# Performance work log

Measured on AMD Instinct MI355X. Metric: run time of the kernel, lower is better.

Reference implementation:

```python
import jax, jax.numpy as jnp
import numpy as np
from jax import lax

B, C, H, W = 8, 64, 128, 128
KS = 3          # kernel size
K = KS * KS     # kernel field = 9
PAD = 1


def conv2d(x, w, b):
    # x: [B,Cin,H,W], w: [Cout,Cin,kh,kw], 'same' 3x3 conv
    y = lax.conv_general_dilated(x, w, window_strides=(1, 1),
                                 padding=((PAD, PAD), (PAD, PAD)),
                                 dimension_numbers=('NCHW', 'OIHW', 'NCHW'))
    return y + b[None, :, None, None]


def modulated_deform_conv(x, offset, mask, weight, bias):
    # x:[B,C,H,W], offset:[B,2K,H,W] (dy,dx per tap), mask:[B,K,H,W]
    Bs, Cin, Hin, Win = x.shape
    off = offset.reshape(Bs, K, 2, Hin, Win)
    ky, kx = jnp.meshgrid(jnp.arange(KS), jnp.arange(KS), indexing='ij')
    ky = ky.reshape(K).astype(x.dtype)   # kernel tap row offsets 0..2
    kx = kx.reshape(K).astype(x.dtype)
    # sampling positions p = p0 + p_k + offset (stride=1, pad=1)
    py = (jnp.arange(Hin, dtype=x.dtype)[None, None, :, None] - PAD
          + ky[None, :, None, None] + off[:, :, 0])            # [B,K,H,W]
    px = (jnp.arange(Win, dtype=x.dtype)[None, None, None, :] - PAD
          + kx[None, :, None, None] + off[:, :, 1])            # [B,K,H,W]

    y0 = jnp.floor(py); x0 = jnp.floor(px)
    ly = py - y0; lx = px - x0                                  # frac parts
    y0i = y0.astype(jnp.int32); x0i = x0.astype(jnp.int32)

    x_flat = x.reshape(Bs, Cin, Hin * Win)

    def gather(iy, ix):
        valid = ((iy >= 0) & (iy < Hin) & (ix >= 0) & (ix < Win))
        flat = (jnp.clip(iy, 0, Hin - 1) * Win + jnp.clip(ix, 0, Win - 1))
        g = jax.vmap(lambda xb, ib: xb[:, ib])(x_flat, flat.reshape(Bs, -1))
        g = g.reshape(Bs, Cin, K, Hin, Win)
        return g * valid[:, None].astype(x.dtype)

    w00 = ((1 - ly) * (1 - lx))[:, None]  # [B,1,K,H,W]
    w01 = ((1 - ly) * lx)[:, None]
    w10 = (ly * (1 - lx))[:, None]
    w11 = (ly * lx)[:, None]

    val = (w00 * gather(y0i, x0i) + w01 * gather(y0i, x0i + 1)
           + w10 * gather(y0i + 1, x0i) + w11 * gather(y0i + 1, x0i + 1))
    val = val * mask[:, None]                                   # modulation
    out = jnp.einsum('ock,bckhw->bohw', weight.reshape(weight.shape[0], Cin, K), val)
    return out + bias[None, :, None, None]


def setup_inputs() -> dict:
    key = jax.random.key(0)
    ks = jax.random.split(key, 7)
    s = 0.05
    return {
        'x': jax.random.normal(ks[0], (B, C, H, W), jnp.float32),
        'w_om': jax.random.normal(ks[1], (3 * K, C, KS, KS), jnp.float32) * s,
        'b_om': jax.random.normal(ks[2], (3 * K,), jnp.float32) * s,
        'w_dc': jax.random.normal(ks[3], (C, C, KS, KS), jnp.float32) * s,
        'b_dc': jax.random.normal(ks[4], (C,), jnp.float32) * s,
        'w_c': jax.random.normal(ks[5], (C, C, KS, KS), jnp.float32) * s,
        'b_c': jax.random.normal(ks[6], (C,), jnp.float32) * s,
    }


def reference(x, w_om, b_om, w_dc, b_dc, w_c, b_c):
    om = conv2d(x, w_om, b_om)                       # [B,3K,H,W]
    offset, mask_raw = om[:, :2 * K], om[:, 2 * K:]
    mask = 2.0 * jax.nn.sigmoid(mask_raw)
    out = modulated_deform_conv(x, offset, mask, w_dc, b_dc)
    act = jnp.where(out > 0, out, 0.2 * out)         # LeakyReLU(0.2)
    return conv2d(act, w_c, b_c) + x
```

## Files before the change

### kernel.cpp

```cpp
#include <hip/hip_runtime.h>
#include <math.h>

#define Bn 8
#define Cn 64
#define Hn 128
#define Wn 128
#define HWn (Hn * Wn)
#define Kn 9

typedef __attribute__((ext_vector_type(8))) short short8;
typedef __attribute__((ext_vector_type(4))) float floatx4;

__device__ __forceinline__ float bf2f(short s) {
  return __uint_as_float(((unsigned)(unsigned short)s) << 16);
}
__device__ __forceinline__ short f2bf(float f) {
  unsigned u = __float_as_uint(f);
  u += 0x7fff + ((u >> 16) & 1);
  return (short)(u >> 16);
}

__global__ __launch_bounds__(256) void k_prep_w(
    const float* __restrict__ w_om, const float* __restrict__ w_dc,
    const float* __restrict__ w_c, short* __restrict__ wt) {
  int idx = blockIdx.x * 256 + threadIdx.x;
  if (idx >= 160 * 576) return;
  int row = idx / 576, k = idx - row * 576;
  int kk = k >> 6, cin = k & 63;
  float v;
  if (row < 32)
    v = (row < 27) ? w_om[(row * 64 + cin) * 9 + kk] : 0.f;
  else if (row < 96)
    v = w_dc[((row - 32) * 64 + cin) * 9 + kk];
  else
    v = w_c[((row - 96) * 64 + cin) * 9 + kk];
  wt[idx] = f2bf(v);
}

__global__ __launch_bounds__(256) void k_prep_x(const float* __restrict__ x,
                                                short* __restrict__ xT) {
  __shared__ float tile[64][129];
  const int h = blockIdx.x, b = blockIdx.y;
  const int tid = threadIdx.x;
  const float* xb = x + (size_t)b * 64 * HWn + h * Wn;
  for (int i = tid; i < 8192; i += 256) {
    int c = i >> 7, w = i & 127;
    tile[c][w] = xb[c * HWn + w];
  }
  __syncthreads();
  short* dst = xT + ((size_t)(b * Hn + h) * Wn) * 64;
  for (int i = tid; i < 2048; i += 256) {
    int w = i >> 4, c4 = (i & 15) * 4;
    short4 o;
    o.x = f2bf(tile[c4 + 0][w]);
    o.y = f2bf(tile[c4 + 1][w]);
    o.z = f2bf(tile[c4 + 2][w]);
    o.w = f2bf(tile[c4 + 3][w]);
    *(short4*)(dst + (size_t)w * 64 + c4) = o;
  }
}

__global__ __launch_bounds__(256) void k_conv_om(
    const short* __restrict__ xT, const short* __restrict__ wt_om,
    const float* __restrict__ b_om, float* __restrict__ offmask) {
  __shared__ short val[64][296];
  const int b = blockIdx.z, h = blockIdx.y, w0 = blockIdx.x * 64;
  const int tid = threadIdx.x;
  const int wave = tid >> 6, lane = tid & 63, quad = lane >> 4, lr = lane & 15;
  const short* xTb = xT + (size_t)b * HWn * 64;

  floatx4 zf = {0.f, 0.f, 0.f, 0.f};
  floatx4 acc0 = zf, acc1 = zf;
  const int m0 = (wave & 1) * 16;
  const int n0 = (wave >> 1) * 32;

  for (int cc = 0; cc < 2; ++cc) {
    __syncthreads();
    for (int j = tid; j < 2304; j += 256) {
      int c8 = (j & 3) * 8;
      int px = (j >> 2) & 63;
      int kk = j >> 8;
      int ky = kk / 3, kx = kk - ky * 3;
      int gy = h + ky - 1, gx = w0 + px + kx - 1;
      short8 v = {0, 0, 0, 0, 0, 0, 0, 0};
      if (gy >= 0 && gy < Hn && gx >= 0 && gx < Wn)
        v = *(const short8*)(xTb + (size_t)(gy * Wn + gx) * 64 + cc * 32 + c8);
      *(short8*)&val[px][kk * 32 + c8] = v;
    }
    __syncthreads();
    const short* wbase = wt_om + cc * 32 + quad * 8;
#pragma unroll
    for (int kk = 0; kk < 9; ++kk) {
      short8 a = *(const short8*)(wbase + (m0 + lr) * 576 + kk * 64);
      short8 bf0 = *(const short8*)&val[n0 + lr][kk * 32 + quad * 8];
      short8 bf1 = *(const short8*)&val[n0 + 16 + lr][kk * 32 + quad * 8];
      acc0 = __builtin_amdgcn_mfma_f32_16x16x32_bf16(a, bf0, acc0, 0, 0, 0);
      acc1 = __builtin_amdgcn_mfma_f32_16x16x32_bf16(a, bf1, acc1, 0, 0, 0);
    }
  }

  float* om_b = offmask + (size_t)b * Kn * 3 * HWn + h * Wn + w0;
#pragma unroll
  for (int nt = 0; nt < 2; ++nt) {
    floatx4 a = nt ? acc1 : acc0;
    int px = n0 + nt * 16 + lr;
#pragma unroll
    for (int r = 0; r < 4; ++r) {
      int cout = m0 + quad * 4 + r;
      if (cout < 27) {
        float v = a[r] + b_om[cout];
        int k, comp;
        if (cout < 18) {
          k = cout >> 1;
          comp = cout & 1;
        } else {
          k = cout - 18;
          comp = 2;
          v = 2.f / (1.f + expf(-v));
        }
        om_b[(size_t)(k * 3 + comp) * HWn + px] = v;
      }
    }
  }
}

__global__ __launch_bounds__(256) void k_deform(
    const short* __restrict__ xT, const float* __restrict__ offmask,
    const short* __restrict__ wt_dc, const float* __restrict__ b_dc,
    short* __restrict__ actT) {
  __shared__ short val[64][296];
  __shared__ int sb[4][9][64];
  __shared__ float sw[4][9][64];
  const int b = blockIdx.z, h = blockIdx.y, w0 = blockIdx.x * 64;
  const int tid = threadIdx.x;
  const int wave = tid >> 6, lane = tid & 63, quad = lane >> 4, lr = lane & 15;
  const short* xTb = xT + (size_t)b * HWn * 64;

  for (int i = tid; i < 576; i += 256) {
    int k = i >> 6, p = i & 63;
    const float* om = offmask + (size_t)(b * Kn + k) * 3 * HWn + h * Wn + w0 + p;
    float offy = om[0];
    float offx = om[HWn];
    float m = om[2 * HWn];
    float py = (float)(h - 1 + (k / 3)) + offy;
    float px_ = (float)(w0 + p - 1 + (k % 3)) + offx;
    float fy = floorf(py), fx = floorf(px_);
    float ly = py - fy, lx = px_ - fx;
    int iy0 = (int)fy, ix0 = (int)fx;
    int iy1 = iy0 + 1, ix1 = ix0 + 1;
    bool vy0 = (iy0 >= 0) && (iy0 < Hn);
    bool vy1 = (iy1 >= 0) && (iy1 < Hn);
    bool vx0 = (ix0 >= 0) && (ix0 < Wn);
    bool vx1 = (ix1 >= 0) && (ix1 < Wn);
    int cy0 = min(max(iy0, 0), Hn - 1), cy1 = min(max(iy1, 0), Hn - 1);
    int cx0 = min(max(ix0, 0), Wn - 1), cx1 = min(max(ix1, 0), Wn - 1);
    sb[0][k][p] = cy0 * Wn + cx0;
    sb[1][k][p] = cy0 * Wn + cx1;
    sb[2][k][p] = cy1 * Wn + cx0;
    sb[3][k][p] = cy1 * Wn + cx1;
    sw[0][k][p] = (vy0 && vx0) ? (1.f - ly) * (1.f - lx) * m : 0.f;
    sw[1][k][p] = (vy0 && vx1) ? (1.f - ly) * lx * m : 0.f;
    sw[2][k][p] = (vy1 && vx0) ? ly * (1.f - lx) * m : 0.f;
    sw[3][k][p] = (vy1 && vx1) ? ly * lx * m : 0.f;
  }

  floatx4 zf = {0.f, 0.f, 0.f, 0.f};
  floatx4 acc[2][2] = {{zf, zf}, {zf, zf}};
  const int m0 = (wave & 1) * 32;
  const int n0 = (wave >> 1) * 32;

  for (int cc = 0; cc < 2; ++cc) {
    __syncthreads();
    for (int j = tid; j < 2304; j += 256) {
      int c8 = (j & 3) * 8;
      int px = (j >> 2) & 63;
      int kk = j >> 8;
      int a0 = sb[0][kk][px], a1 = sb[1][kk][px];
      int a2 = sb[2][kk][px], a3 = sb[3][kk][px];
      float u0 = sw[0][kk][px], u1 = sw[1][kk][px];
      float u2 = sw[2][kk][px], u3 = sw[3][kk][px];
      int cb = cc * 32 + c8;
      short8 q0 = *(const short8*)(xTb + (size_t)a0 * 64 + cb);
      short8 q1 = *(const short8*)(xTb + (size_t)a1 * 64 + cb);
      short8 q2 = *(const short8*)(xTb + (size_t)a2 * 64 + cb);
      short8 q3 = *(const short8*)(xTb + (size_t)a3 * 64 + cb);
      short8 o;
#pragma unroll
      for (int e = 0; e < 8; ++e) {
        float f = u0 * bf2f(q0[e]) + u1 * bf2f(q1[e]) +
                  u2 * bf2f(q2[e]) + u3 * bf2f(q3[e]);
        o[e] = f2bf(f);
      }
      *(short8*)&val[px][kk * 32 + c8] = o;
    }
    __syncthreads();
    const short* wbase = wt_dc + cc * 32 + quad * 8;
#pragma unroll
    for (int kk = 0; kk < 9; ++kk) {
      short8 a0 = *(const short8*)(wbase + (m0 + lr) * 576 + kk * 64);
      short8 a1 = *(const short8*)(wbase + (m0 + 16 + lr) * 576 + kk * 64);
      short8 bf0 = *(const short8*)&val[n0 + lr][kk * 32 + quad * 8];
      short8 bf1 = *(const short8*)&val[n0 + 16 + lr][kk * 32 + quad * 8];
      acc[0][0] = __builtin_amdgcn_mfma_f32_16x16x32_bf16(a0, bf0, acc[0][0], 0, 0, 0);
      acc[0][1] = __builtin_amdgcn_mfma_f32_16x16x32_bf16(a0, bf1, acc[0][1], 0, 0, 0);
      acc[1][0] = __builtin_amdgcn_mfma_f32_16x16x32_bf16(a1, bf0, acc[1][0], 0, 0, 0);
      acc[1][1] = __builtin_amdgcn_mfma_f32_16x16x32_bf16(a1, bf1, acc[1][1], 0, 0, 0);
    }
  }

  short* ab = actT + ((size_t)(b * Hn + h) * Wn) * 64;
#pragma unroll
  for (int mt = 0; mt < 2; ++mt) {
#pragma unroll
    for (int nt = 0; nt < 2; ++nt) {
      int px = n0 + nt * 16 + lr;
      int c0 = m0 + mt * 16 + quad * 4;
      short4 o;
      float v;
      v = acc[mt][nt][0] + b_dc[c0 + 0]; o.x = f2bf(v > 0.f ? v : 0.2f * v);
      v = acc[mt][nt][1] + b_dc[c0 + 1]; o.y = f2bf(v > 0.f ? v : 0.2f * v);
      v = acc[mt][nt][2] + b_dc[c0 + 2]; o.z = f2bf(v > 0.f ? v : 0.2f * v);
      v = acc[mt][nt][3] + b_dc[c0 + 3]; o.w = f2bf(v > 0.f ? v : 0.2f * v);
      *(short4*)(ab + (size_t)(w0 + px) * 64 + c0) = o;
    }
  }
}

__global__ __launch_bounds__(256) void k_conv_out(
    const short* __restrict__ actT, const short* __restrict__ wt_c,
    const float* __restrict__ b_c, const float* __restrict__ x,
    float* __restrict__ out) {
  __shared__ short val[64][296];
  const int b = blockIdx.z, h = blockIdx.y, w0 = blockIdx.x * 64;
  const int tid = threadIdx.x;
  const int wave = tid >> 6, lane = tid & 63, quad = lane >> 4, lr = lane & 15;
  const short* ab = actT + (size_t)b * HWn * 64;

  floatx4 zf = {0.f, 0.f, 0.f, 0.f};
  floatx4 acc[2][2] = {{zf, zf}, {zf, zf}};
  const int m0 = (wave & 1) * 32;
  const int n0 = (wave >> 1) * 32;

  for (int cc = 0; cc < 2; ++cc) {
    __syncthreads();
    for (int j = tid; j < 2304; j += 256) {
      int c8 = (j & 3) * 8;
      int px = (j >> 2) & 63;
      int kk = j >> 8;
      int ky = kk / 3, kx = kk - ky * 3;
      int gy = h + ky - 1, gx = w0 + px + kx - 1;
      short8 v = {0, 0, 0, 0, 0, 0, 0, 0};
      if (gy >= 0 && gy < Hn && gx >= 0 && gx < Wn)
        v = *(const short8*)(ab + (size_t)(gy * Wn + gx) * 64 + cc * 32 + c8);
      *(short8*)&val[px][kk * 32 + c8] = v;
    }
    __syncthreads();
    const short* wbase = wt_c + cc * 32 + quad * 8;
#pragma unroll
    for (int kk = 0; kk < 9; ++kk) {
      short8 a0 = *(const short8*)(wbase + (m0 + lr) * 576 + kk * 64);
      short8 a1 = *(const short8*)(wbase + (m0 + 16 + lr) * 576 + kk * 64);
      short8 bf0 = *(const short8*)&val[n0 + lr][kk * 32 + quad * 8];
      short8 bf1 = *(const short8*)&val[n0 + 16 + lr][kk * 32 + quad * 8];
      acc[0][0] = __builtin_amdgcn_mfma_f32_16x16x32_bf16(a0, bf0, acc[0][0], 0, 0, 0);
      acc[0][1] = __builtin_amdgcn_mfma_f32_16x16x32_bf16(a0, bf1, acc[0][1], 0, 0, 0);
      acc[1][0] = __builtin_amdgcn_mfma_f32_16x16x32_bf16(a1, bf0, acc[1][0], 0, 0, 0);
      acc[1][1] = __builtin_amdgcn_mfma_f32_16x16x32_bf16(a1, bf1, acc[1][1], 0, 0, 0);
    }
  }

#pragma unroll
  for (int mt = 0; mt < 2; ++mt) {
#pragma unroll
    for (int nt = 0; nt < 2; ++nt) {
      int px = n0 + nt * 16 + lr;
#pragma unroll
      for (int r = 0; r < 4; ++r) {
        int cout = m0 + mt * 16 + quad * 4 + r;
        size_t gidx = ((size_t)(b * 64 + cout) * Hn + h) * Wn + w0 + px;
        out[gidx] = acc[mt][nt][r] + b_c[cout] + x[gidx];
      }
    }
  }
}

extern "C" void kernel_launch(void* const* d_in, const int* in_sizes, int n_in,
                              void* d_out, int out_size, void* d_ws,
                              size_t ws_size, hipStream_t stream) {
  const float* x = (const float*)d_in[0];
  const float* w_om = (const float*)d_in[1];
  const float* b_om = (const float*)d_in[2];
  const float* w_dc = (const float*)d_in[3];
  const float* b_dc = (const float*)d_in[4];
  const float* w_c = (const float*)d_in[5];
  const float* b_c = (const float*)d_in[6];
  float* out = (float*)d_out;

  float* offmask = (float*)d_ws;
  short* xT = (short*)(offmask + (size_t)Bn * Kn * 3 * HWn);
  short* actT = xT + (size_t)Bn * HWn * 64;
  short* wt = actT + (size_t)Bn * HWn * 64;

  k_prep_w<<<dim3((160 * 576 + 255) / 256), 256, 0, stream>>>(w_om, w_dc, w_c, wt);
  k_prep_x<<<dim3(Hn, Bn), 256, 0, stream>>>(x, xT);
  k_conv_om<<<dim3(2, Hn, Bn), 256, 0, stream>>>(xT, wt, b_om, offmask);
  k_deform<<<dim3(2, Hn, Bn), 256, 0, stream>>>(xT, offmask, wt + 32 * 576, b_dc, actT);
  k_conv_out<<<dim3(2, Hn, Bn), 256, 0, stream>>>(actT, wt + 96 * 576, b_c, x, out);
}
```

Baseline: 252.1 us.

## Fuse offset conv into deform kernel, split channel layout, use halo tiles for convs

```diff
diff --git a/kernel.cpp b/kernel.cpp
--- a/kernel.cpp
+++ b/kernel.cpp
@@ -7,6 +7,10 @@
 #define Wn 128
 #define HWn (Hn * Wn)
 #define Kn 9
+
+#define XSW 40
+#define XSROW (66 * XSW)
+#define XSCC (3 * XSROW)
 
 typedef __attribute__((ext_vector_type(8))) short short8;
 typedef __attribute__((ext_vector_type(4))) float floatx4;
@@ -38,7 +42,7 @@
 }
 
 __global__ __launch_bounds__(256) void k_prep_x(const float* __restrict__ x,
-                                                short* __restrict__ xT) {
+                                                short* __restrict__ xT2) {
   __shared__ float tile[64][129];
   const int h = blockIdx.x, b = blockIdx.y;
   const int tid = threadIdx.x;
@@ -48,193 +52,209 @@
     tile[c][w] = xb[c * HWn + w];
   }
   __syncthreads();
-  short* dst = xT + ((size_t)(b * Hn + h) * Wn) * 64;
   for (int i = tid; i < 2048; i += 256) {
     int w = i >> 4, c4 = (i & 15) * 4;
+    int half = c4 >> 5, cl = c4 & 31;
     short4 o;
     o.x = f2bf(tile[c4 + 0][w]);
     o.y = f2bf(tile[c4 + 1][w]);
     o.z = f2bf(tile[c4 + 2][w]);
     o.w = f2bf(tile[c4 + 3][w]);
-    *(short4*)(dst + (size_t)w * 64 + c4) = o;
-  }
-}
-
-__global__ __launch_bounds__(256) void k_conv_om(
-    const short* __restrict__ xT, const short* __restrict__ wt_om,
-    const float* __restrict__ b_om, float* __restrict__ offmask) {
-  __shared__ short val[64][296];
+    *(short4*)(xT2 + ((size_t)(b * 2 + half) * HWn + h * Wn + w) * 32 + cl) = o;
+  }
+}
+
+__global__ __launch_bounds__(256, 4) void k_omdef(
+    const short* __restrict__ xT2, const short* __restrict__ wt,
+    const float* __restrict__ b_om, const float* __restrict__ b_dc,
+    short* __restrict__ actT2) {
+  __shared__ __attribute__((aligned(16))) char raw[64 * 296 * 2];
+  short* xs = (short*)raw;
+  float* som = (float*)(raw + XSCC * 2);
+  short(*val)[296] = (short(*)[296])raw;
+
   const int b = blockIdx.z, h = blockIdx.y, w0 = blockIdx.x * 64;
   const int tid = threadIdx.x;
   const int wave = tid >> 6, lane = tid & 63, quad = lane >> 4, lr = lane & 15;
-  const short* xTb = xT + (size_t)b * HWn * 64;
+  const short* xb2 = xT2 + (size_t)b * 2 * HWn * 32;
 
   floatx4 zf = {0.f, 0.f, 0.f, 0.f};
-  floatx4 acc0 = zf, acc1 = zf;
-  const int m0 = (wave & 1) * 16;
+  floatx4 aco0 = zf, aco1 = zf;
+  const int mo0 = (wave & 1) * 16;
   const int n0 = (wave >> 1) * 32;
 
   for (int cc = 0; cc < 2; ++cc) {
-    __syncthreads();
-    for (int j = tid; j < 2304; j += 256) {
+    if (cc) __syncthreads();
+    for (int j = tid; j < 792; j += 256) {
       int c8 = (j & 3) * 8;
-      int px = (j >> 2) & 63;
-      int kk = j >> 8;
-      int ky = kk / 3, kx = kk - ky * 3;
-      int gy = h + ky - 1, gx = w0 + px + kx - 1;
+      int r = j >> 2;
+      int ky = r / 66, p = r - ky * 66;
+      int gy = h + ky - 1, gx = w0 - 1 + p;
       short8 v = {0, 0, 0, 0, 0, 0, 0, 0};
       if (gy >= 0 && gy < Hn && gx >= 0 && gx < Wn)
-        v = *(const short8*)(xTb + (size_t)(gy * Wn + gx) * 64 + cc * 32 + c8);
-      *(short8*)&val[px][kk * 32 + c8] = v;
+        v = *(const short8*)(xb2 + ((size_t)cc * HWn + gy * Wn + gx) * 32 + c8);
+      *(short8*)(xs + ky * XSROW + p * XSW + c8) = v;
     }
     __syncthreads();
-    const short* wbase = wt_om + cc * 32 + quad * 8;
+    const short* wbo = wt + cc * 32 + quad * 8;
 #pragma unroll
     for (int kk = 0; kk < 9; ++kk) {
-      short8 a = *(const short8*)(wbase + (m0 + lr) * 576 + kk * 64);
-      short8 bf0 = *(const short8*)&val[n0 + lr][kk * 32 + quad * 8];
-      short8 bf1 = *(const short8*)&val[n0 + 16 + lr][kk * 32 + quad * 8];
-      acc0 = __builtin_amdgcn_mfma_f32_16x16x32_bf16(a, bf0, acc0, 0, 0, 0);
-      acc1 = __builtin_amdgcn_mfma_f32_16x16x32_bf16(a, bf1, acc1, 0, 0, 0);
-    }
-  }
-
-  float* om_b = offmask + (size_t)b * Kn * 3 * HWn + h * Wn + w0;
+      int ky = kk / 3, kx = kk - ky * 3;
+      short8 a = *(const short8*)(wbo + (mo0 + lr) * 576 + kk * 64);
+      const short* bp = xs + ky * XSROW + kx * XSW + quad * 8;
+      short8 b0 = *(const short8*)(bp + (n0 + lr) * XSW);
+      short8 b1 = *(const short8*)(bp + (n0 + 16 + lr) * XSW);
+      aco0 = __builtin_amdgcn_mfma_f32_16x16x32_bf16(a, b0, aco0, 0, 0, 0);
+      aco1 = __builtin_amdgcn_mfma_f32_16x16x32_bf16(a, b1, aco1, 0, 0, 0);
+    }
+  }
 #pragma unroll
   for (int nt = 0; nt < 2; ++nt) {
-    floatx4 a = nt ? acc1 : acc0;
+    floatx4 a = nt ? aco1 : aco0;
     int px = n0 + nt * 16 + lr;
 #pragma unroll
     for (int r = 0; r < 4; ++r) {
-      int cout = m0 + quad * 4 + r;
-      if (cout < 27) {
-        float v = a[r] + b_om[cout];
-        int k, comp;
-        if (cout < 18) {
-          k = cout >> 1;
-          comp = cout & 1;
-        } else {
-          k = cout - 18;
-          comp = 2;
-          v = 2.f / (1.f + expf(-v));
-        }
-        om_b[(size_t)(k * 3 + comp) * HWn + px] = v;
+      int co = mo0 + quad * 4 + r;
+      if (co < 27) {
+        float v = a[r] + b_om[co];
+        if (co >= 18) v = 2.f / (1.f + expf(-v));
+        som[co * 65 + px] = v;
       }
     }
   }
-}
-
-__global__ __launch_bounds__(256) void k_deform(
-    const short* __restrict__ xT, const float* __restrict__ offmask,
-    const short* __restrict__ wt_dc, const float* __restrict__ b_dc,
-    short* __restrict__ actT) {
-  __shared__ short val[64][296];
-  __shared__ int sb[4][9][64];
-  __shared__ float sw[4][9][64];
-  const int b = blockIdx.z, h = blockIdx.y, w0 = blockIdx.x * 64;
-  const int tid = threadIdx.x;
-  const int wave = tid >> 6, lane = tid & 63, quad = lane >> 4, lr = lane & 15;
-  const short* xTb = xT + (size_t)b * HWn * 64;
-
-  for (int i = tid; i < 576; i += 256) {
-    int k = i >> 6, p = i & 63;
-    const float* om = offmask + (size_t)(b * Kn + k) * 3 * HWn + h * Wn + w0 + p;
-    float offy = om[0];
-    float offx = om[HWn];
-    float m = om[2 * HWn];
-    float py = (float)(h - 1 + (k / 3)) + offy;
-    float px_ = (float)(w0 + p - 1 + (k % 3)) + offx;
-    float fy = floorf(py), fx = floorf(px_);
-    float ly = py - fy, lx = px_ - fx;
-    int iy0 = (int)fy, ix0 = (int)fx;
-    int iy1 = iy0 + 1, ix1 = ix0 + 1;
-    bool vy0 = (iy0 >= 0) && (iy0 < Hn);
-    bool vy1 = (iy1 >= 0) && (iy1 < Hn);
-    bool vx0 = (ix0 >= 0) && (ix0 < Wn);
-    bool vx1 = (ix1 >= 0) && (ix1 < Wn);
-    int cy0 = min(max(iy0, 0), Hn - 1), cy1 = min(max(iy1, 0), Hn - 1);
-    int cx0 = min(max(ix0, 0), Wn - 1), cx1 = min(max(ix1, 0), Wn - 1);
-    sb[0][k][p] = cy0 * Wn + cx0;
-    sb[1][k][p] = cy0 * Wn + cx1;
-    sb[2][k][p] = cy1 * Wn + cx0;
-    sb[3][k][p] = cy1 * Wn + cx1;
-    sw[0][k][p] = (vy0 && vx0) ? (1.f - ly) * (1.f - lx) * m : 0.f;
-    sw[1][k][p] = (vy0 && vx1) ? (1.f - ly) * lx * m : 0.f;
-    sw[2][k][p] = (vy1 && vx0) ? ly * (1.f - lx) * m : 0.f;
-    sw[3][k][p] = (vy1 && vx1) ? ly * lx * m : 0.f;
-  }
-
-  floatx4 zf = {0.f, 0.f, 0.f, 0.f};
+  __syncthreads();
+
+  unsigned pa01[3], pa23[3], pu01[3], pu23[3];
+#pragma unroll
+  for (int t = 0; t < 3; ++t) {
+    int pr = tid + t * 256;
+    if (pr < 576) {
+      int k = pr >> 6, p = pr & 63;
+      float offy = som[(2 * k) * 65 + p];
+      float offx = som[(2 * k + 1) * 65 + p];
+      float m = som[(18 + k) * 65 + p];
+      float py = (float)(h - 1 + (k / 3)) + offy;
+      float px_ = (float)(w0 + p - 1 + (k % 3)) + offx;
+      float fy = floorf(py), fx = floorf(px_);
+      float ly = py - fy, lx = px_ - fx;
+      int iy0 = (int)fy, ix0 = (int)fx;
+      int iy1 = iy0 + 1, ix1 = ix0 + 1;
+      bool vy0 = (iy0 >= 0) && (iy0 < Hn);
+      bool vy1 = (iy1 >= 0) && (iy1 < Hn);
+      bool vx0 = (ix0 >= 0) && (ix0 < Wn);
+      bool vx1 = (ix1 >= 0) && (ix1 < Wn);
+      unsigned cy0 = (unsigned)min(max(iy0, 0), Hn - 1);
+      unsigned cy1 = (unsigned)min(max(iy1, 0), Hn - 1);
+      unsigned cx0 = (unsigned)min(max(ix0, 0), Wn - 1);
+      unsigned cx1 = (unsigned)min(max(ix1, 0), Wn - 1);
+      pa01[t] = (cy0 * Wn + cx0) | ((cy0 * Wn + cx1) << 16);
+      pa23[t] = (cy1 * Wn + cx0) | ((cy1 * Wn + cx1) << 16);
+      float u0 = (vy0 && vx0) ? (1.f - ly) * (1.f - lx) * m : 0.f;
+      float u1 = (vy0 && vx1) ? (1.f - ly) * lx * m : 0.f;
+      float u2 = (vy1 && vx0) ? ly * (1.f - lx) * m : 0.f;
+      float u3 = (vy1 && vx1) ? ly * lx * m : 0.f;
+      pu01[t] = (unsigned)(unsigned short)f2bf(u0) |
+                ((unsigned)(unsigned short)f2bf(u1) << 16);
+      pu23[t] = (unsigned)(unsigned short)f2bf(u2) |
+                ((unsigned)(unsigned short)f2bf(u3) << 16);
+    }
+  }
+  __syncthreads();
+
   floatx4 acc[2][2] = {{zf, zf}, {zf, zf}};
   const int m0 = (wave & 1) * 32;
-  const int n0 = (wave >> 1) * 32;
 
   for (int cc = 0; cc < 2; ++cc) {
+    if (cc) __syncthreads();
+#pragma unroll
+    for (int t = 0; t < 3; ++t) {
+      int pr = tid + t * 256;
+      if (pr < 576) {
+        int k = pr >> 6, p = pr & 63;
+        int a0 = pa01[t] & 0xFFFF, a1 = pa01[t] >> 16;
+        int a2 = pa23[t] & 0xFFFF, a3 = pa23[t] >> 16;
+        float u0 = bf2f((short)(pu01[t] & 0xFFFF));
+        float u1 = bf2f((short)(pu01[t] >> 16));
+        float u2 = bf2f((short)(pu23[t] & 0xFFFF));
+        float u3 = bf2f((short)(pu23[t] >> 16));
+        const short* s0 = xb2 + ((size_t)cc * HWn + a0) * 32;
+        const short* s1 = xb2 + ((size_t)cc * HWn + a1) * 32;
+        const short* s2 = xb2 + ((size_t)cc * HWn + a2) * 32;
+        const short* s3 = xb2 + ((size_t)cc * HWn + a3) * 32;
+#pragma unroll
+        for (int c8 = 0; c8 < 32; c8 += 8) {
+          short8 q0 = *(const short8*)(s0 + c8);
+          short8 q1 = *(const short8*)(s1 + c8);
+          short8 q2 = *(const short8*)(s2 + c8);
+          short8 q3 = *(const short8*)(s3 + c8);
+          short8 o;
+#pragma unroll
+          for (int e = 0; e < 8; ++e) {
+            float f = u0 * bf2f(q0[e]) + u1 * bf2f(q1[e]) +
+                      u2 * bf2f(q2[e]) + u3 * bf2f(q3[e]);
+            o[e] = f2bf(f);
+          }
+          *(short8*)&val[p][k * 32 + c8] = o;
+        }
+      }
+    }
     __syncthreads();
-    for (int j = tid; j < 2304; j += 256) {
-      int c8 = (j & 3) * 8;
-      int px = (j >> 2) & 63;
-      int kk = j >> 8;
-      int a0 = sb[0][kk][px], a1 = sb[1][kk][px];
-      int a2 = sb[2][kk][px], a3 = sb[3][kk][px];
-      float u0 = sw[0][kk][px], u1 = sw[1][kk][px];
-      float u2 = sw[2][kk][px], u3 = sw[3][kk][px];
-      int cb = cc * 32 + c8;
-      short8 q0 = *(const short8*)(xTb + (size_t)a0 * 64 + cb);
-      short8 q1 = *(const short8*)(xTb + (size_t)a1 * 64 + cb);
-      short8 q2 = *(const short8*)(xTb + (size_t)a2 * 64 + cb);
-      short8 q3 = *(const short8*)(xTb + (size_t)a3 * 64 + cb);
-      short8 o;
-#pragma unroll
-      for (int e = 0; e < 8; ++e) {
-        float f = u0 * bf2f(q0[e]) + u1 * bf2f(q1[e]) +
-                  u2 * bf2f(q2[e]) + u3 * bf2f(q3[e]);
-        o[e] = f2bf(f);
-      }
-      *(short8*)&val[px][kk * 32 + c8] = o;
-    }
-    __syncthreads();
-    const short* wbase = wt_dc + cc * 32 + quad * 8;
+    const short* wbd = wt + 32 * 576 + cc * 32 + quad * 8;
 #pragma unroll
     for (int kk = 0; kk < 9; ++kk) {
-      short8 a0 = *(const short8*)(wbase + (m0 + lr) * 576 + kk * 64);
-      short8 a1 = *(const short8*)(wbase + (m0 + 16 + lr) * 576 + kk * 64);
-      short8 bf0 = *(const short8*)&val[n0 + lr][kk * 32 + quad * 8];
-      short8 bf1 = *(const short8*)&val[n0 + 16 + lr][kk * 32 + quad * 8];
-      acc[0][0] = __builtin_amdgcn_mfma_f32_16x16x32_bf16(a0, bf0, acc[0][0], 0, 0, 0);
-      acc[0][1] = __builtin_amdgcn_mfma_f32_16x16x32_bf16(a0, bf1, acc[0][1], 0, 0, 0);
-      acc[1][0] = __builtin_amdgcn_mfma_f32_16x16x32_bf16(a1, bf0, acc[1][0], 0, 0, 0);
-      acc[1][1] = __builtin_amdgcn_mfma_f32_16x16x32_bf16(a1, bf1, acc[1][1], 0, 0, 0);
-    }
-  }
-
-  short* ab = actT + ((size_t)(b * Hn + h) * Wn) * 64;
+      short8 a0 = *(const short8*)(wbd + (m0 + lr) * 576 + kk * 64);
+      short8 a1 = *(const short8*)(wbd + (m0 + 16 + lr) * 576 + kk * 64);
+      short8 b0 = *(const short8*)&val[n0 + lr][kk * 32 + quad * 8];
+      short8 b1 = *(const short8*)&val[n0 + 16 + lr][kk * 32 + quad * 8];
+      acc[0][0] = __builtin_amdgcn_mfma_f32_16x16x32_bf16(a0, b0, acc[0][0], 0, 0, 0);
+      acc[0][1] = __builtin_amdgcn_mfma_f32_16x16x32_bf16(a0, b1, acc[0][1], 0, 0, 0);
+      acc[1][0] = __builtin_amdgcn_mfma_f32_16x16x32_bf16(a1, b0, acc[1][0], 0, 0, 0);
+      acc[1][1] = __builtin_amdgcn_mfma_f32_16x16x32_bf16(a1, b1, acc[1][1], 0, 0, 0);
+    }
+  }
+
 #pragma unroll
   for (int mt = 0; mt < 2; ++mt) {
 #pragma unroll
     for (int nt = 0; nt < 2; ++nt) {
       int px = n0 + nt * 16 + lr;
       int c0 = m0 + mt * 16 + quad * 4;
+      int half = c0 >> 5, cl = c0 & 31;
       short4 o;
       float v;
       v = acc[mt][nt][0] + b_dc[c0 + 0]; o.x = f2bf(v > 0.f ? v : 0.2f * v);
       v = acc[mt][nt][1] + b_dc[c0 + 1]; o.y = f2bf(v > 0.f ? v : 0.2f * v);
       v = acc[mt][nt][2] + b_dc[c0 + 2]; o.z = f2bf(v > 0.f ? v : 0.2f * v);
       v = acc[mt][nt][3] + b_dc[c0 + 3]; o.w = f2bf(v > 0.f ? v : 0.2f * v);
-      *(short4*)(ab + (size_t)(w0 + px) * 64 + c0) = o;
-    }
-  }
-}
-
-__global__ __launch_bounds__(256) void k_conv_out(
-    const short* __restrict__ actT, const short* __restrict__ wt_c,
+      *(short4*)(actT2 +
+                 ((size_t)(b * 2 + half) * HWn + h * Wn + w0 + px) * 32 + cl) = o;
+    }
+  }
+}
+
+__global__ __launch_bounds__(256, 5) void k_conv_out(
+    const short* __restrict__ actT2, const short* __restrict__ wt,
     const float* __restrict__ b_c, const float* __restrict__ x,
     float* __restrict__ out) {
-  __shared__ short val[64][296];
+  __shared__ __attribute__((aligned(16))) short as_[2 * XSCC];
+
   const int b = blockIdx.z, h = blockIdx.y, w0 = blockIdx.x * 64;
   const int tid = threadIdx.x;
   const int wave = tid >> 6, lane = tid & 63, quad = lane >> 4, lr = lane & 15;
-  const short* ab = actT + (size_t)b * HWn * 64;
+  const short* ab2 = actT2 + (size_t)b * 2 * HWn * 32;
+
+  for (int j = tid; j < 1584; j += 256) {
+    int cc = j / 792, r = j - cc * 792;
+    int c8 = (r & 3) * 8;
+    int r2 = r >> 2;
+    int ky = r2 / 66, p = r2 - ky * 66;
+    int gy = h + ky - 1, gx = w0 - 1 + p;
+    short8 v = {0, 0, 0, 0, 0, 0, 0, 0};
+    if (gy >= 0 && gy < Hn && gx >= 0 && gx < Wn)
+      v = *(const short8*)(ab2 + ((size_t)cc * HWn + gy * Wn + gx) * 32 + c8);
+    *(short8*)(as_ + cc * XSCC + ky * XSROW + p * XSW + c8) = v;
+  }
+  __syncthreads();
 
   floatx4 zf = {0.f, 0.f, 0.f, 0.f};
   floatx4 acc[2][2] = {{zf, zf}, {zf, zf}};
@@ -242,30 +262,19 @@
   const int n0 = (wave >> 1) * 32;
 
   for (int cc = 0; cc < 2; ++cc) {
-    __syncthreads();
-    for (int j = tid; j < 2304; j += 256) {
-      int c8 = (j & 3) * 8;
-      int px = (j >> 2) & 63;
-      int kk = j >> 8;
+    const short* wbc = wt + 96 * 576 + cc * 32 + quad * 8;
+#pragma unroll
+    for (int kk = 0; kk < 9; ++kk) {
       int ky = kk / 3, kx = kk - ky * 3;
-      int gy = h + ky - 1, gx = w0 + px + kx - 1;
-      short8 v = {0, 0, 0, 0, 0, 0, 0, 0};
-      if (gy >= 0 && gy < Hn && gx >= 0 && gx < Wn)
-        v = *(const short8*)(ab + (size_t)(gy * Wn + gx) * 64 + cc * 32 + c8);
-      *(short8*)&val[px][kk * 32 + c8] = v;
-    }
-    __syncthreads();
-    const short* wbase = wt_c + cc * 32 + quad * 8;
-#pragma unroll
-    for (int kk = 0; kk < 9; ++kk) {
-      short8 a0 = *(const short8*)(wbase + (m0 + lr) * 576 + kk * 64);
-      short8 a1 = *(const short8*)(wbase + (m0 + 16 + lr) * 576 + kk * 64);
-      short8 bf0 = *(const short8*)&val[n0 + lr][kk * 32 + quad * 8];
-      short8 bf1 = *(const short8*)&val[n0 + 16 + lr][kk * 32 + quad * 8];
-      acc[0][0] = __builtin_amdgcn_mfma_f32_16x16x32_bf16(a0, bf0, acc[0][0], 0, 0, 0);
-      acc[0][1] = __builtin_amdgcn_mfma_f32_16x16x32_bf16(a0, bf1, acc[0][1], 0, 0, 0);
-      acc[1][0] = __builtin_amdgcn_mfma_f32_16x16x32_bf16(a1, bf0, acc[1][0], 0, 0, 0);
-      acc[1][1] = __builtin_amdgcn_mfma_f32_16x16x32_bf16(a1, bf1, acc[1][1], 0, 0, 0);
+      short8 a0 = *(const short8*)(wbc + (m0 + lr) * 576 + kk * 64);
+      short8 a1 = *(const short8*)(wbc + (m0 + 16 + lr) * 576 + kk * 64);
+      const short* bp = as_ + cc * XSCC + ky * XSROW + kx * XSW + quad * 8;
+      short8 b0 = *(const short8*)(bp + (n0 + lr) * XSW);
+      short8 b1 = *(const short8*)(bp + (n0 + 16 + lr) * XSW);
+      acc[0][0] = __builtin_amdgcn_mfma_f32_16x16x32_bf16(a0, b0, acc[0][0], 0, 0, 0);
+      acc[0][1] = __builtin_amdgcn_mfma_f32_16x16x32_bf16(a0, b1, acc[0][1], 0, 0, 0);
+      acc[1][0] = __builtin_amdgcn_mfma_f32_16x16x32_bf16(a1, b0, acc[1][0], 0, 0, 0);
+      acc[1][1] = __builtin_amdgcn_mfma_f32_16x16x32_bf16(a1, b1, acc[1][1], 0, 0, 0);
     }
   }
 
@@ -296,14 +305,12 @@
   const float* b_c = (const float*)d_in[6];
   float* out = (float*)d_out;
 
-  float* offmask = (float*)d_ws;
-  short* xT = (short*)(offmask + (size_t)Bn * Kn * 3 * HWn);
-  short* actT = xT + (size_t)Bn * HWn * 64;
-  short* wt = actT + (size_t)Bn * HWn * 64;
+  short* xT2 = (short*)d_ws;
+  short* actT2 = xT2 + (size_t)Bn * 2 * HWn * 32;
+  short* wt = actT2 + (size_t)Bn * 2 * HWn * 32;
 
   k_prep_w<<<dim3((160 * 576 + 255) / 256), 256, 0, stream>>>(w_om, w_dc, w_c, wt);
-  k_prep_x<<<dim3(Hn, Bn), 256, 0, stream>>>(x, xT);
-  k_conv_om<<<dim3(2, Hn, Bn), 256, 0, stream>>>(xT, wt, b_om, offmask);
-  k_deform<<<dim3(2, Hn, Bn), 256, 0, stream>>>(xT, offmask, wt + 32 * 576, b_dc, actT);
-  k_conv_out<<<dim3(2, Hn, Bn), 256, 0, stream>>>(actT, wt + 96 * 576, b_c, x, out);
-}
+  k_prep_x<<<dim3(Hn, Bn), 256, 0, stream>>>(x, xT2);
+  k_omdef<<<dim3(2, Hn, Bn), 256, 0, stream>>>(xT2, wt, b_om, b_dc, actT2);
+  k_conv_out<<<dim3(2, Hn, Bn), 256, 0, stream>>>(actT2, wt, b_c, x, out);
+}
```

Measured after the change: 261.2 us. 1.04x slower.
